# Kernel optimization log

Measured on AMD Instinct MI355X. Metric: run time of the kernel, lower is better.

## Reference

```python
import jax, jax.numpy as jnp
import numpy as np

B, S, IN_F, OUT_F, RANK = 4, 4096, 4096, 4096, 64

def soft_threshold24(w):
    # 2:4 soft-threshold pruning: groups of 4 along last dim; keep top-2 |w|,
    # soft-threshold by t = 3rd-largest |w| in each group: sign(w)*relu(|w|-t).
    g = w.reshape(w.shape[0], -1, 4)
    a = jnp.abs(g)
    t = jnp.sort(a, axis=-1)[..., 1:2]  # 3rd largest = 2nd smallest of 4
    s = jnp.sign(g) * jnp.maximum(a - t, 0.0)
    return s.reshape(w.shape)

def fake_fp8_mm(a, b):
    # simulated fp8 GEMM per fake_fp8_mm: fp16 operands, fp32 accumulate/output
    return jnp.matmul(a.astype(jnp.float16), b.astype(jnp.float16),
                      preferred_element_type=jnp.float32)

def setup_inputs():
    key = jax.random.key(0)
    k1, k2, k3 = jax.random.split(key, 3)
    x = jax.random.normal(k1, (B, S, IN_F), jnp.float32)
    std_a = float(np.sqrt(2.0 / (IN_F + RANK)))   # xavier_normal_
    std_b = float(np.sqrt(2.0 / (OUT_F + RANK)))
    weight_A = jax.random.normal(k2, (IN_F, RANK), jnp.float32) * std_a
    weight_B = jax.random.normal(k3, (OUT_F, RANK), jnp.float32) * std_b
    bias = jnp.zeros((OUT_F,), jnp.float32)
    scale_A = jnp.float32(1.0)
    scale_B = jnp.float32(1.0)
    return {"x": x, "weight_A": weight_A, "weight_B": weight_B,
            "bias": bias, "scale_A": scale_A, "scale_B": scale_B}

def reference(x, weight_A, weight_B, bias, scale_A, scale_B):
    wA = soft_threshold24(weight_A) * scale_A      # [IN, R], 2:4 sparse along R
    wB = soft_threshold24(weight_B) * scale_B      # [OUT, R], 2:4 sparse along R
    xf = x.reshape(-1, x.shape[-1])                # [N, IN]
    x_proj = fake_fp8_mm(xf, wA)                   # [N, R]   == FP8SparseOp(x, wA.T, None)
    out = fake_fp8_mm(x_proj, wB.T) + bias         # [N, OUT] == FP8SparseOp(x_proj, wB, bias)
    return out.reshape(*x.shape[:-1], OUT_F)
```

## Files before the change

### kernel.cpp

```cpp
#include <hip/hip_runtime.h>
#include <hip/hip_cooperative_groups.h>

namespace cg = cooperative_groups;

#define IN_FEAT 4096
#define OUT_FEAT 4096
#define RANK 64
#define NROWS 16384
#define TM 32
#define BT 512
#define NB 256
#define KC2 256
#define SXS 264
#define BR 256
#define BC 256
#define BS 72
#define KC 256
#define WA_STRIDE 264
#define XP_STRIDE 72

typedef _Float16 half_t;
typedef _Float16 f16x4 __attribute__((ext_vector_type(4)));
typedef _Float16 f16x8 __attribute__((ext_vector_type(8)));
typedef float f32x4 __attribute__((ext_vector_type(4)));

__device__ __forceinline__ f16x4 thr4(float4 v, float s) {
    float a0 = fabsf(v.x), a1 = fabsf(v.y), a2 = fabsf(v.z), a3 = fabsf(v.w);
    float lo1 = fminf(a0, a1), hi1 = fmaxf(a0, a1);
    float lo2 = fminf(a2, a3), hi2 = fmaxf(a2, a3);
    float t = fminf(fmaxf(lo1, lo2), fminf(hi1, hi2));
    f16x4 r;
    r[0] = (half_t)(copysignf(fmaxf(a0 - t, 0.0f), v.x) * s);
    r[1] = (half_t)(copysignf(fmaxf(a1 - t, 0.0f), v.y) * s);
    r[2] = (half_t)(copysignf(fmaxf(a2 - t, 0.0f), v.z) * s);
    r[3] = (half_t)(copysignf(fmaxf(a3 - t, 0.0f), v.w) * s);
    return r;
}

__device__ __forceinline__ f16x4 cvt4(f32x4 v) {
    f16x4 h;
    h[0] = (half_t)v[0]; h[1] = (half_t)v[1];
    h[2] = (half_t)v[2]; h[3] = (half_t)v[3];
    return h;
}

__global__ __launch_bounds__(BT) void coop_v3(
    const float* __restrict__ x, const float* __restrict__ wA,
    const float* __restrict__ wB, const float* __restrict__ bias,
    const float* __restrict__ scaleA, const float* __restrict__ scaleB,
    float* __restrict__ out, half_t* __restrict__ wAT, half_t* __restrict__ wBh,
    half_t* __restrict__ xpw)
{
    __shared__ __align__(16) char pool[BR * BS * 2 + BC * BS * 2];
    __shared__ float biasl[BC];

    int tid = threadIdx.x;
    int bid = blockIdx.x;

    {
        int id = bid * BT + tid;
        if (id < 65536) {
            int row = id >> 4;
            int gq  = id & 15;
            float s = scaleB[0];
            f16x4 h = thr4(*(const float4*)(wB + (size_t)row * RANK + gq * 4), s);
            *(f16x4*)(wBh + (size_t)row * RANK + gq * 4) = h;
        } else if (id < 65536 + 8192) {
            int t2 = id - 65536;
            int c4 = t2 & 15;
            int k8 = t2 >> 4;
            float s = scaleA[0];
            f16x8 vc0, vc1, vc2, vc3;
#pragma unroll
            for (int i = 0; i < 8; ++i) {
                float4 v = *(const float4*)(wA + (size_t)(k8 * 8 + i) * RANK + c4 * 4);
                f16x4 h = thr4(v, s);
                vc0[i] = h[0]; vc1[i] = h[1]; vc2[i] = h[2]; vc3[i] = h[3];
            }
            *(f16x8*)(wAT + (size_t)(c4 * 4 + 0) * IN_FEAT + k8 * 8) = vc0;
            *(f16x8*)(wAT + (size_t)(c4 * 4 + 1) * IN_FEAT + k8 * 8) = vc1;
            *(f16x8*)(wAT + (size_t)(c4 * 4 + 2) * IN_FEAT + k8 * 8) = vc2;
            *(f16x8*)(wAT + (size_t)(c4 * 4 + 3) * IN_FEAT + k8 * 8) = vc3;
        }
    }
    cg::this_grid().sync();

    int wave = tid >> 6;
    int lane = tid & 63;
    int l16  = lane & 15;
    int g    = lane >> 4;

    {
        half_t (*xs)[TM][SXS] = (half_t(*)[TM][SXS])pool;
        int stripe = wave & 1;
        int quad   = wave >> 1;
        int srow = tid >> 4;
        int sseg = tid & 15;

        for (int sub = 0; sub < 2; ++sub) {
            int rowbase = bid * (2 * TM) + sub * TM;
            const float* srcrow = x + (size_t)(rowbase + srow) * IN_FEAT + sseg * 4;

            {
                const f32x4* p = (const f32x4*)(srcrow);
                f32x4 a0 = p[0], a1 = p[16], a2 = p[32], a3 = p[48];
                half_t* dst = &xs[0][srow][sseg * 4];
                *(f16x4*)(dst +   0) = cvt4(a0);
                *(f16x4*)(dst +  64) = cvt4(a1);
                *(f16x4*)(dst + 128) = cvt4(a2);
                *(f16x4*)(dst + 192) = cvt4(a3);
            }
            __syncthreads();

            f32x4 acc = {0, 0, 0, 0};
            const half_t* wcol = wAT + (size_t)(quad * 16 + l16) * IN_FEAT;
            const half_t* arow = &xs[0][stripe * 16 + l16][0];
            const int xsstep = TM * SXS;
            f32x4 ld0, ld1, ld2, ld3;

            for (int c = 0; c < IN_FEAT / KC2; ++c) {
                f16x8 bfr[8];
#pragma unroll
                for (int j = 0; j < 8; ++j)
                    bfr[j] = *(const f16x8*)(wcol + c * KC2 + j * 32 + 8 * g);
                __builtin_amdgcn_sched_barrier(0);
                if (c + 1 < IN_FEAT / KC2) {
                    const f32x4* p = (const f32x4*)(srcrow + (c + 1) * KC2);
                    ld0 = p[0]; ld1 = p[16]; ld2 = p[32]; ld3 = p[48];
                }
                __builtin_amdgcn_sched_barrier(0);

                const half_t* ar = arow + (c & 1) * xsstep;
#pragma unroll
                for (int j = 0; j < 8; ++j) {
                    f16x8 a = *(const f16x8*)(ar + j * 32 + 8 * g);
                    acc = __builtin_amdgcn_mfma_f32_16x16x32_f16(a, bfr[j], acc, 0, 0, 0);
                }
                if (c + 1 < IN_FEAT / KC2) {
                    half_t* dst = &xs[(c + 1) & 1][srow][sseg * 4];
                    *(f16x4*)(dst +   0) = cvt4(ld0);
                    *(f16x4*)(dst +  64) = cvt4(ld1);
                    *(f16x4*)(dst + 128) = cvt4(ld2);
                    *(f16x4*)(dst + 192) = cvt4(ld3);
                }
                __syncthreads();
            }

#pragma unroll
            for (int r = 0; r < 4; ++r)
                xpw[(size_t)(rowbase + stripe * 16 + 4 * g + r) * RANK + quad * 16 + l16]
                    = (half_t)acc[r];
            __syncthreads();
        }
    }
    cg::this_grid().sync();

    {
        half_t (*xps)[BS] = (half_t(*)[BS])pool;
        half_t (*wbs)[BS] = (half_t(*)[BS])(pool + BR * BS * 2);

        int rb = (bid >> 2) * BR;

        {
            int row = tid >> 1, h = tid & 1;
            const half_t* src = xpw + (size_t)(rb + row) * RANK + h * 32;
            f16x8 v0 = *(const f16x8*)(src + 0);
            f16x8 v1 = *(const f16x8*)(src + 8);
            f16x8 v2 = *(const f16x8*)(src + 16);
            f16x8 v3 = *(const f16x8*)(src + 24);
            half_t* dst = &xps[row][h * 32];
            *(f16x8*)(dst + 0)  = v0;
            *(f16x8*)(dst + 8)  = v1;
            *(f16x8*)(dst + 16) = v2;
            *(f16x8*)(dst + 24) = v3;
        }

        int wrow = (wave & 1) * 128;
        int wcol = (wave >> 1) * 64;

        for (int t = 0; t < 4; ++t) {
            int cb = ((bid & 3) * 4 + t) * BC;

            {
                int col = tid >> 1, h = tid & 1;
                const half_t* src = wBh + (size_t)(cb + col) * RANK + h * 32;
                f16x8 v0 = *(const f16x8*)(src + 0);
                f16x8 v1 = *(const f16x8*)(src + 8);
                f16x8 v2 = *(const f16x8*)(src + 16);
                f16x8 v3 = *(const f16x8*)(src + 24);
                half_t* dst = &wbs[col][h * 32];
                *(f16x8*)(dst + 0)  = v0;
                *(f16x8*)(dst + 8)  = v1;
                *(f16x8*)(dst + 16) = v2;
                *(f16x8*)(dst + 24) = v3;
                if (tid < BC) biasl[tid] = bias[cb + tid];
            }
            __syncthreads();

            f16x8 bf0[4], bf1[4];
            float bv[4];
#pragma unroll
            for (int ci = 0; ci < 4; ++ci) {
                int c16 = wcol + ci * 16 + l16;
                bf0[ci] = *(const f16x8*)&wbs[c16][8 * g];
                bf1[ci] = *(const f16x8*)&wbs[c16][32 + 8 * g];
                bv[ci]  = biasl[c16];
            }

            for (int rt = 0; rt < 8; ++rt) {
                const half_t* ar = &xps[wrow + rt * 16 + l16][0];
                f16x8 a0 = *(const f16x8*)(ar + 8 * g);
                f16x8 a1 = *(const f16x8*)(ar + 32 + 8 * g);
                int row0 = rb + wrow + rt * 16 + 4 * g;
#pragma unroll
                for (int ci = 0; ci < 4; ++ci) {
                    f32x4 acc2 = {0, 0, 0, 0};
                    acc2 = __builtin_amdgcn_mfma_f32_16x16x32_f16(a0, bf0[ci], acc2, 0, 0, 0);
                    acc2 = __builtin_amdgcn_mfma_f32_16x16x32_f16(a1, bf1[ci], acc2, 0, 0, 0);
                    int col = cb + wcol + ci * 16 + l16;
#pragma unroll
                    for (int r = 0; r < 4; ++r)
                        out[(size_t)(row0 + r) * OUT_FEAT + col] = acc2[r] + bv[ci];
                }
            }
            __syncthreads();
        }
    }
}

__global__ __launch_bounds__(256) void fused_kernel(
    const float* __restrict__ x, const float* __restrict__ wA,
    const float* __restrict__ wB, const float* __restrict__ bias,
    const float* __restrict__ scaleA, const float* __restrict__ scaleB,
    float* __restrict__ out)
{
    __shared__ __align__(16) half_t wAsT[RANK][WA_STRIDE];
    __shared__ float xp_part[2][TM][XP_STRIDE];
    __shared__ __align__(16) half_t xp[TM][XP_STRIDE];

    int tid  = threadIdx.x;
    int wave = tid >> 6;
    int lane = tid & 63;
    int l16  = lane & 15;
    int g    = lane >> 4;
    int rowbase = blockIdx.x * TM;
    int stripe  = wave & 1;
    int ks      = wave >> 1;

    float sA = scaleA[0];
    float sB = scaleB[0];

    const float* xrow = x + (size_t)(rowbase + stripe * 16 + l16) * IN_FEAT;
    f32x4 acc[4] = {f32x4{0,0,0,0}, f32x4{0,0,0,0}, f32x4{0,0,0,0}, f32x4{0,0,0,0}};

    for (int chunk = 0; chunk < IN_FEAT / KC; ++chunk) {
        int k0 = chunk * KC;
#pragma unroll
        for (int pp = 0; pp < 2; ++pp) {
            int p = tid + pp * 256;
            int q = p & 15;
            int r = p >> 4;
            f16x8 vc0, vc1, vc2, vc3;
#pragma unroll
            for (int i = 0; i < 8; ++i) {
                float4 v = *(const float4*)(wA + (size_t)(k0 + 8 * r + i) * RANK + 4 * q);
                f16x4 h = thr4(v, sA);
                vc0[i] = h[0]; vc1[i] = h[1]; vc2[i] = h[2]; vc3[i] = h[3];
            }
            *(f16x8*)&wAsT[4 * q + 0][8 * r] = vc0;
            *(f16x8*)&wAsT[4 * q + 1][8 * r] = vc1;
            *(f16x8*)&wAsT[4 * q + 2][8 * r] = vc2;
            *(f16x8*)&wAsT[4 * q + 3][8 * r] = vc3;
        }
        __syncthreads();

#pragma unroll
        for (int it = 0; it < 4; ++it) {
            int kloc = ks * 128 + it * 32;
            float4 xa = *(const float4*)(xrow + k0 + kloc + 8 * g);
            float4 xb = *(const float4*)(xrow + k0 + kloc + 8 * g + 4);
            f16x8 a;
            a[0] = (half_t)xa.x; a[1] = (half_t)xa.y; a[2] = (half_t)xa.z; a[3] = (half_t)xa.w;
            a[4] = (half_t)xb.x; a[5] = (half_t)xb.y; a[6] = (half_t)xb.z; a[7] = (half_t)xb.w;
#pragma unroll
            for (int f = 0; f < 4; ++f) {
                f16x8 b = *(const f16x8*)&wAsT[16 * f + l16][kloc + 8 * g];
                acc[f] = __builtin_amdgcn_mfma_f32_16x16x32_f16(a, b, acc[f], 0, 0, 0);
            }
        }
        __syncthreads();
    }

#pragma unroll
    for (int f = 0; f < 4; ++f)
#pragma unroll
        for (int r = 0; r < 4; ++r)
            xp_part[ks][stripe * 16 + 4 * g + r][16 * f + l16] = acc[f][r];
    __syncthreads();

#pragma unroll
    for (int i = 0; i < (TM * RANK) / 256; ++i) {
        int e = i * 256 + tid;
        int r = e >> 6, c = e & 63;
        xp[r][c] = (half_t)(xp_part[0][r][c] + xp_part[1][r][c]);
    }
    __syncthreads();

    {
        const half_t* xprow = &xp[stripe * 16 + l16][0];
        f16x8 a0 = *(const f16x8*)(xprow + 8 * g);
        f16x8 a1 = *(const f16x8*)(xprow + 32 + 8 * g);

        int cb0 = ks * (OUT_FEAT / 2);
        for (int cb = cb0; cb < cb0 + OUT_FEAT / 2; cb += 16) {
            int col = cb + l16;
            const float* wp = wB + (size_t)col * RANK;
            float4 w00 = *(const float4*)(wp + 8 * g);
            float4 w01 = *(const float4*)(wp + 8 * g + 4);
            float4 w10 = *(const float4*)(wp + 32 + 8 * g);
            float4 w11 = *(const float4*)(wp + 32 + 8 * g + 4);
            f16x4 b00 = thr4(w00, sB), b01 = thr4(w01, sB);
            f16x4 b10 = thr4(w10, sB), b11 = thr4(w11, sB);
            f16x8 b0, b1;
            b0[0]=b00[0]; b0[1]=b00[1]; b0[2]=b00[2]; b0[3]=b00[3];
            b0[4]=b01[0]; b0[5]=b01[1]; b0[6]=b01[2]; b0[7]=b01[3];
            b1[0]=b10[0]; b1[1]=b10[1]; b1[2]=b10[2]; b1[3]=b10[3];
            b1[4]=b11[0]; b1[5]=b11[1]; b1[6]=b11[2]; b1[7]=b11[3];

            f32x4 acc2 = {0, 0, 0, 0};
            acc2 = __builtin_amdgcn_mfma_f32_16x16x32_f16(a0, b0, acc2, 0, 0, 0);
            acc2 = __builtin_amdgcn_mfma_f32_16x16x32_f16(a1, b1, acc2, 0, 0, 0);
            float bv = bias[col];
#pragma unroll
            for (int r = 0; r < 4; ++r)
                out[(size_t)(rowbase + stripe * 16 + 4 * g + r) * OUT_FEAT + col] = acc2[r] + bv;
        }
    }
}

extern "C" void kernel_launch(void* const* d_in, const int* in_sizes, int n_in,
                              void* d_out, int out_size, void* d_ws, size_t ws_size,
                              hipStream_t stream) {
    const float* x      = (const float*)d_in[0];
    const float* wA     = (const float*)d_in[1];
    const float* wB     = (const float*)d_in[2];
    const float* bias   = (const float*)d_in[3];
    const float* scaleA = (const float*)d_in[4];
    const float* scaleB = (const float*)d_in[5];
    float* out = (float*)d_out;

    const size_t WS_V3 = (size_t)RANK * IN_FEAT * 2
                       + (size_t)OUT_FEAT * RANK * 2
                       + (size_t)NROWS * RANK * 2;

    bool launched = false;
    if (ws_size >= WS_V3 && d_ws != nullptr) {
        half_t* wAT = (half_t*)d_ws;
        half_t* wBh = wAT + (size_t)RANK * IN_FEAT;
        half_t* xpw = wBh + (size_t)OUT_FEAT * RANK;
        void* args[] = {(void*)&x, (void*)&wA, (void*)&wB, (void*)&bias,
                        (void*)&scaleA, (void*)&scaleB, (void*)&out,
                        (void*)&wAT, (void*)&wBh, (void*)&xpw};
        hipError_t err = hipLaunchCooperativeKernel((void*)coop_v3,
                                                    dim3(NB), dim3(BT),
                                                    args, 0, stream);
        launched = (err == hipSuccess);
    }
    if (!launched) {
        fused_kernel<<<NROWS / TM, 256, 0, stream>>>(x, wA, wB, bias, scaleA, scaleB, out);
    }
}
```

Baseline: 221.2 us.

## Restage second GEMM output through LDS for coalesced float4 row stores

Phase two of the cooperative kernel now swaps the MFMA operand order so each lane produces a row-contiguous 4-float fragment. The 16x256 output tile goes through a double-buffered LDS row buffer, then each wave writes full rows with 128-bit coalesced global stores instead of scattered scalar stores. wB fragments and bias are loaded straight into registers, and x_proj rows are prefetched from global one step ahead, so the old wB/x_proj LDS staging is gone. The cost is a __syncthreads per 16-row step and extra LDS traffic, in exchange for far more efficient writes of the large fp32 output.

```diff
diff --git a/kernel.cpp b/kernel.cpp
--- a/kernel.cpp
+++ b/kernel.cpp
@@ -14,7 +14,7 @@
 #define SXS 264
 #define BR 256
 #define BC 256
-#define BS 72
+#define RBS 264
 #define KC 256
 #define WA_STRIDE 264
 #define XP_STRIDE 72
@@ -51,8 +51,7 @@
     float* __restrict__ out, half_t* __restrict__ wAT, half_t* __restrict__ wBh,
     half_t* __restrict__ xpw)
 {
-    __shared__ __align__(16) char pool[BR * BS * 2 + BC * BS * 2];
-    __shared__ float biasl[BC];
+    __shared__ __align__(16) char pool[2 * TM * SXS * 2];
 
     int tid = threadIdx.x;
     int bid = blockIdx.x;
@@ -156,74 +155,64 @@
     cg::this_grid().sync();
 
     {
-        half_t (*xps)[BS] = (half_t(*)[BS])pool;
-        half_t (*wbs)[BS] = (half_t(*)[BS])(pool + BR * BS * 2);
+        float (*rowbuf)[16][RBS] = (float(*)[16][RBS])pool;
 
         int rb = (bid >> 2) * BR;
-
-        {
-            int row = tid >> 1, h = tid & 1;
-            const half_t* src = xpw + (size_t)(rb + row) * RANK + h * 32;
-            f16x8 v0 = *(const f16x8*)(src + 0);
-            f16x8 v1 = *(const f16x8*)(src + 8);
-            f16x8 v2 = *(const f16x8*)(src + 16);
-            f16x8 v3 = *(const f16x8*)(src + 24);
-            half_t* dst = &xps[row][h * 32];
-            *(f16x8*)(dst + 0)  = v0;
-            *(f16x8*)(dst + 8)  = v1;
-            *(f16x8*)(dst + 16) = v2;
-            *(f16x8*)(dst + 24) = v3;
-        }
-
-        int wrow = (wave & 1) * 128;
-        int wcol = (wave >> 1) * 64;
+        int ci0 = 2 * wave;
 
         for (int t = 0; t < 4; ++t) {
             int cb = ((bid & 3) * 4 + t) * BC;
 
+            f16x8 wf00, wf01, wf10, wf11;
+            f32x4 bv0, bv1;
             {
-                int col = tid >> 1, h = tid & 1;
-                const half_t* src = wBh + (size_t)(cb + col) * RANK + h * 32;
-                f16x8 v0 = *(const f16x8*)(src + 0);
-                f16x8 v1 = *(const f16x8*)(src + 8);
-                f16x8 v2 = *(const f16x8*)(src + 16);
-                f16x8 v3 = *(const f16x8*)(src + 24);
-                half_t* dst = &wbs[col][h * 32];
-                *(f16x8*)(dst + 0)  = v0;
-                *(f16x8*)(dst + 8)  = v1;
-                *(f16x8*)(dst + 16) = v2;
-                *(f16x8*)(dst + 24) = v3;
-                if (tid < BC) biasl[tid] = bias[cb + tid];
-            }
-            __syncthreads();
-
-            f16x8 bf0[4], bf1[4];
-            float bv[4];
-#pragma unroll
-            for (int ci = 0; ci < 4; ++ci) {
-                int c16 = wcol + ci * 16 + l16;
-                bf0[ci] = *(const f16x8*)&wbs[c16][8 * g];
-                bf1[ci] = *(const f16x8*)&wbs[c16][32 + 8 * g];
-                bv[ci]  = biasl[c16];
-            }
-
-            for (int rt = 0; rt < 8; ++rt) {
-                const half_t* ar = &xps[wrow + rt * 16 + l16][0];
-                f16x8 a0 = *(const f16x8*)(ar + 8 * g);
-                f16x8 a1 = *(const f16x8*)(ar + 32 + 8 * g);
-                int row0 = rb + wrow + rt * 16 + 4 * g;
-#pragma unroll
-                for (int ci = 0; ci < 4; ++ci) {
-                    f32x4 acc2 = {0, 0, 0, 0};
-                    acc2 = __builtin_amdgcn_mfma_f32_16x16x32_f16(a0, bf0[ci], acc2, 0, 0, 0);
-                    acc2 = __builtin_amdgcn_mfma_f32_16x16x32_f16(a1, bf1[ci], acc2, 0, 0, 0);
-                    int col = cb + wcol + ci * 16 + l16;
-#pragma unroll
-                    for (int r = 0; r < 4; ++r)
-                        out[(size_t)(row0 + r) * OUT_FEAT + col] = acc2[r] + bv[ci];
-                }
-            }
-            __syncthreads();
+                const half_t* w0 = wBh + (size_t)(cb + ci0 * 16 + l16) * RANK;
+                const half_t* w1 = wBh + (size_t)(cb + (ci0 + 1) * 16 + l16) * RANK;
+                wf00 = *(const f16x8*)(w0 + 8 * g);
+                wf01 = *(const f16x8*)(w0 + 32 + 8 * g);
+                wf10 = *(const f16x8*)(w1 + 8 * g);
+                wf11 = *(const f16x8*)(w1 + 32 + 8 * g);
+                bv0 = *(const f32x4*)(bias + cb + ci0 * 16 + 4 * g);
+                bv1 = *(const f32x4*)(bias + cb + (ci0 + 1) * 16 + 4 * g);
+            }
+
+            const half_t* xpr = xpw + (size_t)(rb + l16) * RANK;
+            f16x8 a0 = *(const f16x8*)(xpr + 8 * g);
+            f16x8 a1 = *(const f16x8*)(xpr + 32 + 8 * g);
+
+            for (int rt = 0; rt < 16; ++rt) {
+                f16x8 n0, n1;
+                if (rt + 1 < 16) {
+                    const half_t* xq = xpw + (size_t)(rb + (rt + 1) * 16 + l16) * RANK;
+                    n0 = *(const f16x8*)(xq + 8 * g);
+                    n1 = *(const f16x8*)(xq + 32 + 8 * g);
+                }
+                __builtin_amdgcn_sched_barrier(0);
+
+                f32x4 c0 = {0, 0, 0, 0}, c1 = {0, 0, 0, 0};
+                c0 = __builtin_amdgcn_mfma_f32_16x16x32_f16(wf00, a0, c0, 0, 0, 0);
+                c0 = __builtin_amdgcn_mfma_f32_16x16x32_f16(wf01, a1, c0, 0, 0, 0);
+                c1 = __builtin_amdgcn_mfma_f32_16x16x32_f16(wf10, a0, c1, 0, 0, 0);
+                c1 = __builtin_amdgcn_mfma_f32_16x16x32_f16(wf11, a1, c1, 0, 0, 0);
+                c0[0] += bv0[0]; c0[1] += bv0[1]; c0[2] += bv0[2]; c0[3] += bv0[3];
+                c1[0] += bv1[0]; c1[1] += bv1[1]; c1[2] += bv1[2]; c1[3] += bv1[3];
+
+                float* rbw = &rowbuf[rt & 1][l16][0];
+                *(f32x4*)(rbw + ci0 * 16 + 4 * g)       = c0;
+                *(f32x4*)(rbw + (ci0 + 1) * 16 + 4 * g) = c1;
+                __syncthreads();
+
+                {
+                    const float* r0 = &rowbuf[rt & 1][wave][4 * lane];
+                    const float* r1 = &rowbuf[rt & 1][wave + 8][4 * lane];
+                    f32x4 s0 = *(const f32x4*)r0;
+                    f32x4 s1 = *(const f32x4*)r1;
+                    *(f32x4*)&out[(size_t)(rb + rt * 16 + wave) * OUT_FEAT + cb + 4 * lane] = s0;
+                    *(f32x4*)&out[(size_t)(rb + rt * 16 + wave + 8) * OUT_FEAT + cb + 4 * lane] = s1;
+                }
+
+                a0 = n0; a1 = n1;
+            }
         }
     }
 }
```

Result: slower. 226.0 us (median of 2 runs) (+2.2%).
